# Optimization experiments

Hardware: AMD Instinct MI355X
Metric: run time of the kernel (lower is better)

## Reference

```python
import jax, jax.numpy as jnp
import numpy as np

L, S, B, E, H, FF = 2048, 2048, 4, 1024, 16, 4096
HD = E // H
EPS = 1e-5


def _ln(x, g, b):
    mu = jnp.mean(x, axis=-1, keepdims=True)
    var = jnp.mean(jnp.square(x - mu), axis=-1, keepdims=True)
    return (x - mu) * jax.lax.rsqrt(var + EPS) * g + b


def _mha(xq, xk, xv, Wq, bq, Wk, bk, Wv, bv, Wo, bo, mask):
    l, bsz, e = xq.shape
    s = xk.shape[0]
    q = (xq @ Wq.T + bq).reshape(l, bsz, H, HD)
    k = (xk @ Wk.T + bk).reshape(s, bsz, H, HD)
    v = (xv @ Wv.T + bv).reshape(s, bsz, H, HD)
    scores = jnp.einsum('lbhd,sbhd->bhls', q, k) / (float(HD) ** 0.5)
    if mask is not None:
        scores = scores + mask  # broadcast (L,S) over (B,H,L,S)
    w = jax.nn.softmax(scores, axis=-1)
    out = jnp.einsum('bhls,sbhd->lbhd', w, v).reshape(l, bsz, e)
    return out @ Wo.T + bo


def setup_inputs() -> dict:
    key = jax.random.key(0)
    ks = jax.random.split(key, 32)
    sc = 0.02
    d = {
        'tgt': jax.random.normal(ks[0], (L, B, E), jnp.float32),
        'memory': jax.random.normal(ks[1], (S, B, E), jnp.float32),
        'tgt_mask': jnp.where(jnp.triu(jnp.ones((L, L), bool), k=1), -jnp.inf, 0.0).astype(jnp.float32),
    }
    def lin(i, out_d, in_d):
        return jax.random.normal(ks[i], (out_d, in_d), jnp.float32) * sc, jnp.zeros((out_d,), jnp.float32)
    for pfx, base in (('sa', 2), ('ca', 6)):
        for j, nm in enumerate(('Wq', 'Wk', 'Wv', 'Wo')):
            W, b = lin(base + j, E, E)
            d[f'{pfx}_{nm}'] = W
            d[f'{pfx}_b{nm[1]}'] = b
    d['W1'], d['b1'] = lin(10, FF, E)
    d['W2'], d['b2'] = lin(11, E, FF)
    for i, nm in enumerate(('ln1', 'ln2', 'ln3')):
        d[f'{nm}_g'] = jnp.ones((E,), jnp.float32)
        d[f'{nm}_b'] = jnp.zeros((E,), jnp.float32)
    return d


def reference(tgt, memory, tgt_mask,
              sa_Wq, sa_bq, sa_Wk, sa_bk, sa_Wv, sa_bv, sa_Wo, sa_bo,
              ca_Wq, ca_bq, ca_Wk, ca_bk, ca_Wv, ca_bv, ca_Wo, ca_bo,
              W1, b1, W2, b2,
              ln1_g, ln1_b, ln2_g, ln2_b, ln3_g, ln3_b):
    # masked self-attention + residual + norm1
    sa = _mha(tgt, tgt, tgt, sa_Wq, sa_bq, sa_Wk, sa_bk, sa_Wv, sa_bv, sa_Wo, sa_bo, tgt_mask)
    x = _ln(tgt + sa, ln1_g, ln1_b)
    # cross-attention + residual + norm2
    ca = _mha(x, memory, memory, ca_Wq, ca_bq, ca_Wk, ca_bk, ca_Wv, ca_bv, ca_Wo, ca_bo, None)
    x = _ln(x + ca, ln2_g, ln2_b)
    # FFN + residual + norm3 (dropout = identity in eval)
    ffn = jax.nn.relu(x @ W1.T + b1) @ W2.T + b2
    return _ln(x + ffn, ln3_g, ln3_b)
```

## Files before the change

kernel.cpp:

```cpp
#include <hip/hip_runtime.h>
#include <cstdint>

typedef unsigned short u16;
typedef __bf16 bf16x8 __attribute__((ext_vector_type(8)));
typedef float f32x4 __attribute__((ext_vector_type(4)));

#define L_ 2048
#define S_ 2048
#define B_ 4
#define E_ 1024
#define H_ 16
#define FF_ 4096
#define M_ (L_*B_)

#define QK_SCALE 0.18033688f

__device__ __forceinline__ unsigned f2bf(float f) {
  unsigned u = __float_as_uint(f);
  return (u + 0x7fffu + ((u >> 16) & 1u)) >> 16;
}
__device__ __forceinline__ float bflo(unsigned u){ return __uint_as_float(u << 16); }
__device__ __forceinline__ float bfhi(unsigned u){ return __uint_as_float(u & 0xffff0000u); }

struct CvtSeg { const float* src; u16* dst; int blk_end; };
struct CvtTab { CvtSeg s[6]; };

__global__ __launch_bounds__(256) void cvt_all(CvtTab t, int nseg) {
  const int blk = blockIdx.x;
  int k = 0;
  while (k < nseg - 1 && blk >= t.s[k].blk_end) k++;
  const int b0 = (k == 0) ? 0 : t.s[k-1].blk_end;
  const int off = (blk - b0) * 1024 + threadIdx.x * 4;
  float4 f = *(const float4*)(t.s[k].src + off);
  uint2 u;
  u.x = f2bf(f.x) | (f2bf(f.y) << 16);
  u.y = f2bf(f.z) | (f2bf(f.w) << 16);
  *(uint2*)(t.s[k].dst + off) = u;
}

struct GTab { u16* o[3]; const float* b[3]; float sc[3]; };

__device__ __forceinline__ void gl_lds16(const u16* g, u16* l) {
  __builtin_amdgcn_global_load_lds(
      (const __attribute__((address_space(1))) unsigned int*)g,
      (__attribute__((address_space(3))) unsigned int*)l, 16, 0, 0);
}

#define RAW_BARRIER() do { \
  asm volatile("" ::: "memory"); \
  __builtin_amdgcn_s_barrier(); \
  asm volatile("" ::: "memory"); \
} while (0)

template<int RELU, int NG>
__global__ __launch_bounds__(256, 2) void gemm_bt(
    const u16* __restrict__ A,
    const u16* __restrict__ Bw,
    GTab t, int K, int N)
{
  __shared__ __align__(16) u16 As[128*32];
  __shared__ __align__(16) u16 Bs[128*32];
  const int tid  = threadIdx.x;
  const int lane = tid & 63;
  const int quad = lane >> 4;
  const int l16  = lane & 15;
  const int wave = tid >> 6;
  const int wm = (wave & 1) << 6;
  const int wn = (wave >> 1) << 6;
  const int bm = blockIdx.y << 7;
  const int bn = blockIdx.x << 7;

  const int grp = (NG > 1) ? ((int)blockIdx.x >> 3) : 0;
  u16* Cb = t.o[grp];
  const float* bias = t.b[grp];
  const float scale = t.sc[grp];
  const int ld = (NG > 1) ? 1024 : N;

  const int e0 = tid << 3;
  const int r0 = e0 >> 5;
  const int c0 = e0 & 31;
  const u16* a0 = A  + (size_t)(bm + r0)      * K + c0;
  const u16* a1 = A  + (size_t)(bm + r0 + 64) * K + c0;
  const u16* b0 = Bw + (size_t)(bn + r0)      * K + c0;
  const u16* b1 = Bw + (size_t)(bn + r0 + 64) * K + c0;

  f32x4 acc[4][4];
  #pragma unroll
  for (int i = 0; i < 4; i++)
    #pragma unroll
    for (int j = 0; j < 4; j++)
      acc[i][j] = (f32x4){0.f, 0.f, 0.f, 0.f};

  for (int k0 = 0; k0 < K; k0 += 32) {
    __syncthreads();
    gl_lds16(a0, As + e0);
    gl_lds16(a1, As + e0 + 2048);
    gl_lds16(b0, Bs + e0);
    gl_lds16(b1, Bs + e0 + 2048);
    a0 += 32; a1 += 32; b0 += 32; b1 += 32;
    __syncthreads();

    bf16x8 af[4], bfv[4];
    #pragma unroll
    for (int tt = 0; tt < 4; tt++) {
      af[tt]  = *(const bf16x8*)(As + ((wm + tt*16 + l16) << 5) + (quad << 3));
      bfv[tt] = *(const bf16x8*)(Bs + ((wn + tt*16 + l16) << 5) + (quad << 3));
    }
    #pragma unroll
    for (int mt = 0; mt < 4; mt++)
      #pragma unroll
      for (int nt = 0; nt < 4; nt++)
        acc[mt][nt] = __builtin_amdgcn_mfma_f32_16x16x32_bf16(af[mt], bfv[nt], acc[mt][nt], 0, 0, 0);
  }

  #pragma unroll
  for (int nt = 0; nt < 4; nt++) {
    const int col = bn + wn + nt*16 + l16;
    const int ocol = (NG > 1) ? (col & 1023) : col;
    const float bv = bias[ocol];
    #pragma unroll
    for (int mt = 0; mt < 4; mt++) {
      #pragma unroll
      for (int i = 0; i < 4; i++) {
        const int row = bm + wm + mt*16 + quad*4 + i;
        float v = (acc[mt][nt][i] + bv) * scale;
        if (RELU) v = fmaxf(v, 0.0f);
        Cb[(size_t)row * ld + ocol] = (u16)f2bf(v);
      }
    }
  }
}

template<int RELU, int NG>
__global__ __launch_bounds__(512, 2) void gemm256(
    const u16* __restrict__ A,
    const u16* __restrict__ Bw,
    GTab t, int K, int N)
{
  extern __shared__ __align__(16) u16 LDs[];
  const int tid  = threadIdx.x;
  const int lane = tid & 63;
  const int quad = lane >> 4;
  const int l16  = lane & 15;
  const int w    = tid >> 6;
  const int wm   = w >> 2;
  const int wn   = w & 3;
  const int bm = blockIdx.y << 8;
  const int bn = blockIdx.x << 8;

  const int grp = (NG > 1) ? ((int)blockIdx.x >> 2) : 0;
  u16* Cb = t.o[grp];
  const float* bias = t.b[grp];
  const float scale = t.sc[grp];
  const int ld = (NG > 1) ? 1024 : N;

  const int srow = (w << 4) + (lane >> 2);
  const int cg8  = ((lane & 3) ^ ((lane >> 3) & 3)) << 3;
  const u16* pa0 = A  + (size_t)(bm + srow) * K + cg8;
  const u16* pa1 = pa0 + (size_t)128 * K;
  const u16* pb0 = Bw + (size_t)(bn + srow) * K + cg8;
  const u16* pb1 = pb0 + (size_t)128 * K;
  const int wds = w << 9;

  const int swz  = (quad ^ ((l16 >> 1) & 3)) << 3;
  const int aoff = ((wm << 7) + l16) * 32 + swz;
  const int boff = 8192 + ((wn << 6) + l16) * 32 + swz;

  f32x4 acc[8][4];
  #pragma unroll
  for (int i = 0; i < 8; i++)
    #pragma unroll
    for (int j = 0; j < 4; j++)
      acc[i][j] = (f32x4){0.f, 0.f, 0.f, 0.f};

  const int nk = K >> 5;

  #pragma unroll
  for (int kt = 0; kt < 3; kt++) {
    const int sb = kt << 14;
    gl_lds16(pa0 + kt*32, LDs + sb + wds);
    gl_lds16(pa1 + kt*32, LDs + sb + 4096  + wds);
    gl_lds16(pb0 + kt*32, LDs + sb + 8192  + wds);
    gl_lds16(pb1 + kt*32, LDs + sb + 12288 + wds);
  }
  pa0 += 96; pa1 += 96; pb0 += 96; pb1 += 96;
  asm volatile("s_waitcnt vmcnt(8)" ::: "memory");
  RAW_BARRIER();

  for (int it = 0; it < nk; ++it) {
    const int rb = (it & 3) << 14;
    const int sb = ((it + 3) & 3) << 14;

    bf16x8 bfr[4], afr[4];
    #pragma unroll
    for (int nt = 0; nt < 4; nt++)
      bfr[nt] = *(const bf16x8*)(LDs + rb + boff + nt*512);
    #pragma unroll
    for (int mt = 0; mt < 4; mt++)
      afr[mt] = *(const bf16x8*)(LDs + rb + aoff + mt*512);
    gl_lds16(pa0, LDs + sb + wds);
    gl_lds16(pa1, LDs + sb + 4096 + wds);
    RAW_BARRIER();
    __builtin_amdgcn_s_setprio(1);
    #pragma unroll
    for (int mt = 0; mt < 4; mt++)
      #pragma unroll
      for (int nt = 0; nt < 4; nt++)
        acc[mt][nt] = __builtin_amdgcn_mfma_f32_16x16x32_bf16(afr[mt], bfr[nt], acc[mt][nt], 0, 0, 0);
    __builtin_amdgcn_s_setprio(0);
    RAW_BARRIER();

    #pragma unroll
    for (int mt = 0; mt < 4; mt++)
      afr[mt] = *(const bf16x8*)(LDs + rb + aoff + (4 + mt)*512);
    gl_lds16(pb0, LDs + sb + 8192  + wds);
    gl_lds16(pb1, LDs + sb + 12288 + wds);
    asm volatile("s_waitcnt vmcnt(8)" ::: "memory");
    RAW_BARRIER();
    __builtin_amdgcn_s_setprio(1);
    #pragma unroll
    for (int mt = 0; mt < 4; mt++)
      #pragma unroll
      for (int nt = 0; nt < 4; nt++)
        acc[4 + mt][nt] = __builtin_amdgcn_mfma_f32_16x16x32_bf16(afr[mt], bfr[nt], acc[4 + mt][nt], 0, 0, 0);
    __builtin_amdgcn_s_setprio(0);
    RAW_BARRIER();

    if (it + 4 < nk) { pa0 += 32; pa1 += 32; pb0 += 32; pb1 += 32; }
  }

  #pragma unroll
  for (int nt = 0; nt < 4; nt++) {
    const int col = bn + (wn << 6) + nt*16 + l16;
    const int ocol = (NG > 1) ? (col & 1023) : col;
    const float bv = bias[ocol];
    #pragma unroll
    for (int mt = 0; mt < 8; mt++) {
      #pragma unroll
      for (int i = 0; i < 4; i++) {
        const int row = bm + (wm << 7) + mt*16 + quad*4 + i;
        float v = (acc[mt][nt][i] + bv) * scale;
        if (RELU) v = fmaxf(v, 0.0f);
        Cb[(size_t)row * ld + ocol] = (u16)f2bf(v);
      }
    }
  }
}

__global__ __launch_bounds__(256) void transpose_v(
    const u16* __restrict__ V, u16* __restrict__ Vt)
{
  const int t = threadIdx.x;
  const int lane = t & 63;
  const int w = t >> 6;
  const int bh = blockIdx.y;
  const int b = bh >> 4, h = bh & 15;
  const int l = (blockIdx.x << 6) + lane;
  const size_t vrow = ((size_t)l * B_ + b) * E_ + h * 64;
  #pragma unroll
  for (int g = 0; g < 2; g++) {
    const int d0 = w * 8 + g * 32;
    uint4 u = *(const uint4*)(V + vrow + d0);
    u16 e[8];
    e[0] = u.x & 0xffff; e[1] = u.x >> 16;
    e[2] = u.y & 0xffff; e[3] = u.y >> 16;
    e[4] = u.z & 0xffff; e[5] = u.z >> 16;
    e[6] = u.w & 0xffff; e[7] = u.w >> 16;
    #pragma unroll
    for (int j = 0; j < 8; j++)
      Vt[(size_t)(bh * 64 + d0 + j) * S_ + l] = e[j];
  }
}

template<int CAUSAL>
__global__ __launch_bounds__(256, 4) void attn_mfma(
    const u16* __restrict__ Q,
    const u16* __restrict__ Kg,
    const u16* __restrict__ Vt,
    u16* __restrict__ O,
    int Skv)
{
  __shared__ __align__(16) u16 Tile[16384];
  const int tid  = threadIdx.x;
  const int lane = tid & 63;
  const int w    = tid >> 6;
  const int l16  = lane & 15;
  const int quad = lane >> 4;
  const int bh = blockIdx.x;
  const int b = bh >> 4, h = bh & 15;
  const int y = blockIdx.y;
  const int q0 = (CAUSAL ? ((y < 8) ? (15 - 2*y) : (2*y - 16)) : y) << 7;
  const int wq = q0 + w*32;

  bf16x8 qf[2][2];
  #pragma unroll
  for (int h2 = 0; h2 < 2; h2++) {
    const size_t qoff = ((size_t)(wq + h2*16 + l16) * B_ + b) * E_ + h*64;
    qf[h2][0] = *(const bf16x8*)(Q + qoff + quad*8);
    qf[h2][1] = *(const bf16x8*)(Q + qoff + 32 + quad*8);
  }

  f32x4 oacc[2][4];
  #pragma unroll
  for (int h2 = 0; h2 < 2; h2++)
    #pragma unroll
    for (int i = 0; i < 4; i++) oacc[h2][i] = (f32x4){0.f,0.f,0.f,0.f};
  float lsum[2] = {0.f, 0.f};

  const int lrow = lane >> 3;
  const int lchunk = (lane & 7) ^ lrow;
  const u16* kp = Kg + ((size_t)(16*w + lrow) * B_ + b) * E_ + h*64 + lchunk*8;
  const u16* vp = Vt + (size_t)(bh*64 + 16*w + lrow) * Skv + lchunk*8;
  const size_t kRow8 = (size_t)8 * B_ * E_;
  const size_t kTile = (size_t)64 * B_ * E_;
  u16* ldsK = Tile + w*1024;
  u16* ldsV = Tile + 4096 + w*1024;

  const int pbase = 8192 + w*2048;
  int aKV[2], aW[4];
  #pragma unroll
  for (int kh = 0; kh < 2; kh++)
    aKV[kh] = l16*64 + (((kh*4 + quad) ^ (l16 & 7)) << 3);
  #pragma unroll
  for (int st = 0; st < 4; st++)
    aW[st] = pbase + l16*64 +
             ((((st*2) + (quad >> 1)) ^ (l16 & 7)) << 3) + ((quad & 1) << 2);

  const int send = CAUSAL ? (q0 + 128) : Skv;
  for (int s0 = 0; s0 < send; s0 += 64) {
    __syncthreads();
    gl_lds16(kp,         ldsK);
    gl_lds16(kp + kRow8, ldsK + 512);
    gl_lds16(vp,         ldsV);
    gl_lds16(vp + 8*Skv, ldsV + 512);
    kp += kTile; vp += 64;
    __syncthreads();

    if (CAUSAL && s0 >= wq + 32) continue;

    f32x4 sacc[2][4];
    #pragma unroll
    for (int h2 = 0; h2 < 2; h2++)
      #pragma unroll
      for (int st = 0; st < 4; st++) sacc[h2][st] = (f32x4){0.f,0.f,0.f,0.f};
    #pragma unroll
    for (int kh = 0; kh < 2; kh++)
      #pragma unroll
      for (int st = 0; st < 4; st++) {
        bf16x8 kf = *(const bf16x8*)(Tile + aKV[kh] + st*1024);
        sacc[0][st] = __builtin_amdgcn_mfma_f32_16x16x32_bf16(kf, qf[0][kh], sacc[0][st], 0, 0, 0);
        sacc[1][st] = __builtin_amdgcn_mfma_f32_16x16x32_bf16(kf, qf[1][kh], sacc[1][st], 0, 0, 0);
      }

    #pragma unroll
    for (int h2 = 0; h2 < 2; h2++) {
      float p[16];
      #pragma unroll
      for (int st = 0; st < 4; st++)
        #pragma unroll
        for (int r = 0; r < 4; r++) p[st*4+r] = sacc[h2][st][r];
      if (CAUSAL && s0 + 63 > wq + h2*16) {
        const int qa = wq + h2*16 + l16;
        #pragma unroll
        for (int st = 0; st < 4; st++)
          #pragma unroll
          for (int r = 0; r < 4; r++)
            if (s0 + st*16 + quad*4 + r > qa) p[st*4+r] = -3e38f;
      }
      #pragma unroll
      for (int i = 0; i < 16; i++) p[i] = exp2f(p[i]);
      float s01 = (p[0]+p[1]) + (p[2]+p[3]);
      float s23 = (p[4]+p[5]) + (p[6]+p[7]);
      float s45 = (p[8]+p[9]) + (p[10]+p[11]);
      float s67 = (p[12]+p[13]) + (p[14]+p[15]);
      lsum[h2] += (s01+s23) + (s45+s67);

      #pragma unroll
      for (int st = 0; st < 4; st++) {
        uint2 d;
        d.x = __builtin_amdgcn_perm(__float_as_uint(p[st*4+1]), __float_as_uint(p[st*4+0]), 0x07060302u);
        d.y = __builtin_amdgcn_perm(__float_as_uint(p[st*4+3]), __float_as_uint(p[st*4+2]), 0x07060302u);
        *(uint2*)(Tile + aW[st] + h2*1024) = d;
      }
    }

    #pragma unroll
    for (int kh = 0; kh < 2; kh++) {
      bf16x8 pf[2];
      #pragma unroll
      for (int h2 = 0; h2 < 2; h2++)
        pf[h2] = *(const bf16x8*)(Tile + pbase + h2*1024 + aKV[kh]);
      #pragma unroll
      for (int dt = 0; dt < 4; dt++) {
        bf16x8 vf = *(const bf16x8*)(Tile + 4096 + aKV[kh] + dt*1024);
        #pragma unroll
        for (int h2 = 0; h2 < 2; h2++)
          oacc[h2][dt] = __builtin_amdgcn_mfma_f32_16x16x32_bf16(pf[h2], vf, oacc[h2][dt], 0, 0, 0);
      }
    }
  }

  #pragma unroll
  for (int h2 = 0; h2 < 2; h2++) {
    float rs = lsum[h2];
    rs += __shfl_xor(rs, 16);
    rs += __shfl_xor(rs, 32);
    const float inv = 1.0f / rs;
    #pragma unroll
    for (int r = 0; r < 4; r++) {
      const float li = __shfl(inv, (quad << 2) + r);
      const int qg = wq + h2*16 + quad*4 + r;
      const size_t orow = ((size_t)qg * B_ + b) * E_ + h*64;
      #pragma unroll
      for (int dt = 0; dt < 4; dt++)
        O[orow + dt*16 + l16] = (u16)f2bf(oacc[h2][dt][r] * li);
    }
  }
}

template<int RF32>
__global__ __launch_bounds__(256) void add_ln(
    const u16* __restrict__ X,
    const float* __restrict__ Rf, const u16* __restrict__ Rb,
    const float* __restrict__ g, const float* __restrict__ be,
    float* __restrict__ outF, u16* __restrict__ outB)
{
  const int row = blockIdx.x;
  const int tid = threadIdx.x;
  const size_t base = (size_t)row * E_;
  uint2 xu = *(const uint2*)(X + base + tid*4);
  float x0 = bflo(xu.x), x1 = bfhi(xu.x), x2 = bflo(xu.y), x3 = bfhi(xu.y);
  float r0, r1, r2, r3;
  if (RF32) {
    float4 rv = *(const float4*)(Rf + base + tid*4);
    r0 = rv.x; r1 = rv.y; r2 = rv.z; r3 = rv.w;
  } else {
    uint2 ru = *(const uint2*)(Rb + base + tid*4);
    r0 = bflo(ru.x); r1 = bfhi(ru.x); r2 = bflo(ru.y); r3 = bfhi(ru.y);
  }
  const float v0 = x0 + r0, v1 = x1 + r1, v2 = x2 + r2, v3 = x3 + r3;
  float s  = v0 + v1 + v2 + v3;
  float s2 = v0*v0 + v1*v1 + v2*v2 + v3*v3;
  #pragma unroll
  for (int off = 32; off >= 1; off >>= 1) {
    s  += __shfl_down(s,  off);
    s2 += __shfl_down(s2, off);
  }
  __shared__ float ps[4], ps2[4];
  const int wv = tid >> 6, lane = tid & 63;
  if (lane == 0) { ps[wv] = s; ps2[wv] = s2; }
  __syncthreads();
  const float ts  = ps[0] + ps[1] + ps[2] + ps[3];
  const float ts2 = ps2[0] + ps2[1] + ps2[2] + ps2[3];
  const float mu  = ts * (1.0f / E_);
  const float var = ts2 * (1.0f / E_) - mu * mu;
  const float rsq = rsqrtf(var + 1e-5f);
  float4 gv = *(const float4*)(g  + tid*4);
  float4 bv = *(const float4*)(be + tid*4);
  const float o0 = (v0 - mu) * rsq * gv.x + bv.x;
  const float o1 = (v1 - mu) * rsq * gv.y + bv.y;
  const float o2 = (v2 - mu) * rsq * gv.z + bv.z;
  const float o3 = (v3 - mu) * rsq * gv.w + bv.w;
  if (outF) {
    float4 ov; ov.x = o0; ov.y = o1; ov.z = o2; ov.w = o3;
    *(float4*)(outF + base + tid*4) = ov;
  }
  if (outB) {
    uint2 u;
    u.x = f2bf(o0) | (f2bf(o1) << 16);
    u.y = f2bf(o2) | (f2bf(o3) << 16);
    *(uint2*)(outB + base + tid*4) = u;
  }
}

extern "C" void kernel_launch(void* const* d_in, const int* in_sizes, int n_in,
                              void* d_out, int out_size, void* d_ws, size_t ws_size,
                              hipStream_t stream) {
  (void)in_sizes; (void)n_in; (void)out_size; (void)ws_size;
  const float* tgt  = (const float*)d_in[0];
  const float* mem  = (const float*)d_in[1];
  const float* saWq = (const float*)d_in[3];  const float* sabq = (const float*)d_in[4];
  const float* saWk = (const float*)d_in[5];  const float* sabk = (const float*)d_in[6];
  const float* saWv = (const float*)d_in[7];  const float* sabv = (const float*)d_in[8];
  const float* saWo = (const float*)d_in[9];  const float* sabo = (const float*)d_in[10];
  const float* caWq = (const float*)d_in[11]; const float* cabq = (const float*)d_in[12];
  const float* caWk = (const float*)d_in[13]; const float* cabk = (const float*)d_in[14];
  const float* caWv = (const float*)d_in[15]; const float* cabv = (const float*)d_in[16];
  const float* caWo = (const float*)d_in[17]; const float* cabo = (const float*)d_in[18];
  const float* W1   = (const float*)d_in[19]; const float* b1   = (const float*)d_in[20];
  const float* W2   = (const float*)d_in[21]; const float* b2   = (const float*)d_in[22];
  const float* ln1g = (const float*)d_in[23]; const float* ln1b = (const float*)d_in[24];
  const float* ln2g = (const float*)d_in[25]; const float* ln2b = (const float*)d_in[26];
  const float* ln3g = (const float*)d_in[27]; const float* ln3b = (const float*)d_in[28];
  float* out = (float*)d_out;

  static bool attr_done = false;
  if (!attr_done) {
    (void)hipFuncSetAttribute(reinterpret_cast<const void*>(&gemm256<0,3>),
                              hipFuncAttributeMaxDynamicSharedMemorySize, 131072);
    (void)hipFuncSetAttribute(reinterpret_cast<const void*>(&gemm256<0,2>),
                              hipFuncAttributeMaxDynamicSharedMemorySize, 131072);
    (void)hipFuncSetAttribute(reinterpret_cast<const void*>(&gemm256<1,1>),
                              hipFuncAttributeMaxDynamicSharedMemorySize, 131072);
    attr_done = true;
  }

  char* wsp = (char*)d_ws;
  const size_t MB16 = (size_t)16 * 1024 * 1024;
  u16* A  = (u16*)(wsp + 0 * MB16);
  u16* Cq = (u16*)(wsp + 1 * MB16);
  u16* Bm = (u16*)(wsp + 2 * MB16);
  u16* Dk = (u16*)(wsp + 3 * MB16);
  u16* Ev = (u16*)(wsp + 4 * MB16);
  u16* Ff = (u16*)(wsp + 5 * MB16);
  u16* wS = (u16*)(wsp + 6 * MB16);
  u16* hb = Cq;
  const int MEG = 1024 * 1024;

  dim3 blk(256);
  dim3 blk512(512);
  dim3 g8(8, 64);
  dim3 gQKV256(12, 32);
  dim3 gKV256(8, 32);
  dim3 gFF256(16, 32);
  dim3 ga(B_*H_, L_/128);
  dim3 gt(S_/64, B_*H_);

  auto gt1 = [](u16* o, const float* bi, float s) {
    GTab t{}; t.o[0]=o; t.o[1]=o; t.o[2]=o; t.b[0]=bi; t.b[1]=bi; t.b[2]=bi;
    t.sc[0]=s; t.sc[1]=s; t.sc[2]=s; return t;
  };

  {
    CvtTab t{};
    t.s[0] = {tgt,  A,        8192};
    t.s[1] = {mem,  Bm,       16384};
    t.s[2] = {saWq, wS,       17408};
    t.s[3] = {saWk, wS + MEG,   18432};
    t.s[4] = {saWv, wS + 2*MEG, 19456};
    t.s[5] = {saWo, wS + 3*MEG, 20480};
    cvt_all<<<20480, blk, 0, stream>>>(t, 6);
  }

  {
    GTab t{};
    t.o[0]=Cq; t.o[1]=Dk; t.o[2]=Ev;
    t.b[0]=sabq; t.b[1]=sabk; t.b[2]=sabv;
    t.sc[0]=QK_SCALE; t.sc[1]=1.f; t.sc[2]=1.f;
    gemm256<0,3><<<gQKV256, blk512, 131072, stream>>>(A, wS, t, E_, 3*E_);
  }
  transpose_v<<<gt, blk, 0, stream>>>(Ev, Ff);
  attn_mfma<1><<<ga, blk, 0, stream>>>(Cq, Dk, Ff, Cq, S_);
  gemm_bt<0,1><<<g8, blk, 0, stream>>>(Cq, wS + 3*MEG, gt1(Ff, sabo, 1.f), E_, E_);
  add_ln<1><<<M_, blk, 0, stream>>>(Ff, tgt, nullptr, ln1g, ln1b, nullptr, A);

  {
    CvtTab t{};
    t.s[0] = {caWq, wS,        1024};
    t.s[1] = {caWk, wS + MEG,    2048};
    t.s[2] = {caWv, wS + 2*MEG,  3072};
    t.s[3] = {caWo, wS + 3*MEG,  4096};
    cvt_all<<<4096, blk, 0, stream>>>(t, 4);
  }

  gemm_bt<0,1><<<g8, blk, 0, stream>>>(A, wS, gt1(Cq, cabq, QK_SCALE), E_, E_);
  {
    GTab t{};
    t.o[0]=Dk; t.o[1]=Ev; t.o[2]=Ev;
    t.b[0]=cabk; t.b[1]=cabv; t.b[2]=cabv;
    t.sc[0]=1.f; t.sc[1]=1.f; t.sc[2]=1.f;
    gemm256<0,2><<<gKV256, blk512, 131072, stream>>>(Bm, wS + MEG, t, E_, 2*E_);
  }
  transpose_v<<<gt, blk, 0, stream>>>(Ev, Ff);
  attn_mfma<0><<<ga, blk, 0, stream>>>(Cq, Dk, Ff, Cq, S_);
  gemm_bt<0,1><<<g8, blk, 0, stream>>>(Cq, wS + 3*MEG, gt1(Ff, cabo, 1.f), E_, E_);
  add_ln<0><<<M_, blk, 0, stream>>>(Ff, nullptr, A, ln2g, ln2b, nullptr, A);

  {
    CvtTab t{};
    t.s[0] = {W1, wS, 4096};
    cvt_all<<<4096, blk, 0, stream>>>(t, 1);
  }
  gemm256<1,1><<<gFF256, blk512, 131072, stream>>>(A, wS, gt1(hb, b1, 1.f), E_, FF_);
  {
    CvtTab t{};
    t.s[0] = {W2, wS, 4096};
    cvt_all<<<4096, blk, 0, stream>>>(t, 1);
  }
  gemm_bt<0,1><<<g8, blk, 0, stream>>>(hb, wS, gt1(Ff, b2, 1.f), FF_, E_);
  add_ln<0><<<M_, blk, 0, stream>>>(Ff, nullptr, A, ln3g, ln3b, out, nullptr);
}
```

Baseline: 824.3 us.

## Replace N=1024 GEMMs with pipelined 256x128 tile kernel using swizzled LDS

Swaps the simple 128x128 single-buffered gemm_bt kernel, used for the output projections, the cross-attention Q projection and the FFN down-projection, for a new 256x128 tile kernel with 512 threads. The new kernel keeps a three-stage ring of LDS buffers filled asynchronously with global_load_lds, XOR-swizzles the LDS layout to avoid bank conflicts, and splits each k-step into two MFMA phases with setprio. The aim is to hide global-load latency behind the matrix math and cut the per-k-step barrier stalls of the old kernel. The larger tile halves the grid to 256 blocks, which may leave some compute units underused.

```diff
diff --git a/kernel.cpp b/kernel.cpp
--- a/kernel.cpp
+++ b/kernel.cpp
@@ -51,85 +51,6 @@
   __builtin_amdgcn_s_barrier(); \
   asm volatile("" ::: "memory"); \
 } while (0)
-
-template<int RELU, int NG>
-__global__ __launch_bounds__(256, 2) void gemm_bt(
-    const u16* __restrict__ A,
-    const u16* __restrict__ Bw,
-    GTab t, int K, int N)
-{
-  __shared__ __align__(16) u16 As[128*32];
-  __shared__ __align__(16) u16 Bs[128*32];
-  const int tid  = threadIdx.x;
-  const int lane = tid & 63;
-  const int quad = lane >> 4;
-  const int l16  = lane & 15;
-  const int wave = tid >> 6;
-  const int wm = (wave & 1) << 6;
-  const int wn = (wave >> 1) << 6;
-  const int bm = blockIdx.y << 7;
-  const int bn = blockIdx.x << 7;
-
-  const int grp = (NG > 1) ? ((int)blockIdx.x >> 3) : 0;
-  u16* Cb = t.o[grp];
-  const float* bias = t.b[grp];
-  const float scale = t.sc[grp];
-  const int ld = (NG > 1) ? 1024 : N;
-
-  const int e0 = tid << 3;
-  const int r0 = e0 >> 5;
-  const int c0 = e0 & 31;
-  const u16* a0 = A  + (size_t)(bm + r0)      * K + c0;
-  const u16* a1 = A  + (size_t)(bm + r0 + 64) * K + c0;
-  const u16* b0 = Bw + (size_t)(bn + r0)      * K + c0;
-  const u16* b1 = Bw + (size_t)(bn + r0 + 64) * K + c0;
-
-  f32x4 acc[4][4];
-  #pragma unroll
-  for (int i = 0; i < 4; i++)
-    #pragma unroll
-    for (int j = 0; j < 4; j++)
-      acc[i][j] = (f32x4){0.f, 0.f, 0.f, 0.f};
-
-  for (int k0 = 0; k0 < K; k0 += 32) {
-    __syncthreads();
-    gl_lds16(a0, As + e0);
-    gl_lds16(a1, As + e0 + 2048);
-    gl_lds16(b0, Bs + e0);
-    gl_lds16(b1, Bs + e0 + 2048);
-    a0 += 32; a1 += 32; b0 += 32; b1 += 32;
-    __syncthreads();
-
-    bf16x8 af[4], bfv[4];
-    #pragma unroll
-    for (int tt = 0; tt < 4; tt++) {
-      af[tt]  = *(const bf16x8*)(As + ((wm + tt*16 + l16) << 5) + (quad << 3));
-      bfv[tt] = *(const bf16x8*)(Bs + ((wn + tt*16 + l16) << 5) + (quad << 3));
-    }
-    #pragma unroll
-    for (int mt = 0; mt < 4; mt++)
-      #pragma unroll
-      for (int nt = 0; nt < 4; nt++)
-        acc[mt][nt] = __builtin_amdgcn_mfma_f32_16x16x32_bf16(af[mt], bfv[nt], acc[mt][nt], 0, 0, 0);
-  }
-
-  #pragma unroll
-  for (int nt = 0; nt < 4; nt++) {
-    const int col = bn + wn + nt*16 + l16;
-    const int ocol = (NG > 1) ? (col & 1023) : col;
-    const float bv = bias[ocol];
-    #pragma unroll
-    for (int mt = 0; mt < 4; mt++) {
-      #pragma unroll
-      for (int i = 0; i < 4; i++) {
-        const int row = bm + wm + mt*16 + quad*4 + i;
-        float v = (acc[mt][nt][i] + bv) * scale;
-        if (RELU) v = fmaxf(v, 0.0f);
-        Cb[(size_t)row * ld + ocol] = (u16)f2bf(v);
-      }
-    }
-  }
-}
 
 template<int RELU, int NG>
 __global__ __launch_bounds__(512, 2) void gemm256(
@@ -242,6 +163,112 @@
         float v = (acc[mt][nt][i] + bv) * scale;
         if (RELU) v = fmaxf(v, 0.0f);
         Cb[(size_t)row * ld + ocol] = (u16)f2bf(v);
+      }
+    }
+  }
+}
+
+template<int RELU>
+__global__ __launch_bounds__(512, 2) void gemm256n(
+    const u16* __restrict__ A,
+    const u16* __restrict__ Bw,
+    const float* __restrict__ bias,
+    u16* __restrict__ C,
+    float scale, int K, int N)
+{
+  extern __shared__ __align__(16) u16 LDs[];
+  const int tid  = threadIdx.x;
+  const int lane = tid & 63;
+  const int quad = lane >> 4;
+  const int l16  = lane & 15;
+  const int w    = tid >> 6;
+  const int wm   = w >> 1;
+  const int wn   = w & 1;
+  const int bm = blockIdx.y << 8;
+  const int bn = blockIdx.x << 7;
+
+  const int srow = (w << 4) + (lane >> 2);
+  const int cg8  = ((lane & 3) ^ ((lane >> 3) & 3)) << 3;
+  const u16* pa0 = A  + (size_t)(bm + srow) * K + cg8;
+  const u16* pa1 = pa0 + (size_t)128 * K;
+  const u16* pb0 = Bw + (size_t)(bn + srow) * K + cg8;
+  const int wds = w << 9;
+
+  const int swz  = (quad ^ ((l16 >> 1) & 3)) << 3;
+  const int aoff = ((wm << 6) + l16) * 32 + swz;
+  const int boff = 8192 + ((wn << 6) + l16) * 32 + swz;
+
+  f32x4 acc[4][4];
+  #pragma unroll
+  for (int i = 0; i < 4; i++)
+    #pragma unroll
+    for (int j = 0; j < 4; j++)
+      acc[i][j] = (f32x4){0.f, 0.f, 0.f, 0.f};
+
+  const int nk = K >> 5;
+
+  #pragma unroll
+  for (int kt = 0; kt < 2; kt++) {
+    const int sb = kt * 12288;
+    gl_lds16(pa0 + kt*32, LDs + sb + wds);
+    gl_lds16(pa1 + kt*32, LDs + sb + 4096 + wds);
+    gl_lds16(pb0 + kt*32, LDs + sb + 8192 + wds);
+  }
+  pa0 += 64; pa1 += 64; pb0 += 64;
+  asm volatile("s_waitcnt vmcnt(3)" ::: "memory");
+  RAW_BARRIER();
+
+  int rb = 0, sb = 24576;
+  for (int it = 0; it < nk; ++it) {
+    bf16x8 bfr[4], afr0, afr1;
+    #pragma unroll
+    for (int nt = 0; nt < 4; nt++)
+      bfr[nt] = *(const bf16x8*)(LDs + rb + boff + nt*512);
+    afr0 = *(const bf16x8*)(LDs + rb + aoff);
+    afr1 = *(const bf16x8*)(LDs + rb + aoff + 512);
+    gl_lds16(pa0, LDs + sb + wds);
+    gl_lds16(pa1, LDs + sb + 4096 + wds);
+    RAW_BARRIER();
+    __builtin_amdgcn_s_setprio(1);
+    #pragma unroll
+    for (int nt = 0; nt < 4; nt++) {
+      acc[0][nt] = __builtin_amdgcn_mfma_f32_16x16x32_bf16(afr0, bfr[nt], acc[0][nt], 0, 0, 0);
+      acc[1][nt] = __builtin_amdgcn_mfma_f32_16x16x32_bf16(afr1, bfr[nt], acc[1][nt], 0, 0, 0);
+    }
+    __builtin_amdgcn_s_setprio(0);
+    RAW_BARRIER();
+
+    afr0 = *(const bf16x8*)(LDs + rb + aoff + 1024);
+    afr1 = *(const bf16x8*)(LDs + rb + aoff + 1536);
+    gl_lds16(pb0, LDs + sb + 8192 + wds);
+    asm volatile("s_waitcnt vmcnt(3)" ::: "memory");
+    RAW_BARRIER();
+    __builtin_amdgcn_s_setprio(1);
+    #pragma unroll
+    for (int nt = 0; nt < 4; nt++) {
+      acc[2][nt] = __builtin_amdgcn_mfma_f32_16x16x32_bf16(afr0, bfr[nt], acc[2][nt], 0, 0, 0);
+      acc[3][nt] = __builtin_amdgcn_mfma_f32_16x16x32_bf16(afr1, bfr[nt], acc[3][nt], 0, 0, 0);
+    }
+    __builtin_amdgcn_s_setprio(0);
+    RAW_BARRIER();
+
+    if (it + 3 < nk) { pa0 += 32; pa1 += 32; pb0 += 32; }
+    rb += 12288; if (rb == 36864) rb = 0;
+    sb += 12288; if (sb == 36864) sb = 0;
+  }
+
+  #pragma unroll
+  for (int nt = 0; nt < 4; nt++) {
+    const int col = bn + (wn << 6) + nt*16 + l16;
+    const float bv = bias[col];
+    #pragma unroll
+    for (int mt = 0; mt < 4; mt++) {
+      #pragma unroll
+      for (int i = 0; i < 4; i++) {
+        const int row = bm + (wm << 6) + mt*16 + quad*4 + i;
+        float v = (acc[mt][nt][i] + bv) * scale;
+        if (RELU) v = fmaxf(v, 0.0f);
+        C[(size_t)row * N + col] = (u16)f2bf(v);
       }
     }
   }
@@ -502,6 +529,8 @@
                               hipFuncAttributeMaxDynamicSharedMemorySize, 131072);
     (void)hipFuncSetAttribute(reinterpret_cast<const void*>(&gemm256<1,1>),
                               hipFuncAttributeMaxDynamicSharedMemorySize, 131072);
+    (void)hipFuncSetAttribute(reinterpret_cast<const void*>(&gemm256n<0>),
+                              hipFuncAttributeMaxDynamicSharedMemorySize, 73728);
     attr_done = true;
   }
 
@@ -519,17 +548,12 @@
 
   dim3 blk(256);
   dim3 blk512(512);
-  dim3 g8(8, 64);
+  dim3 gN1(8, 32);
   dim3 gQKV256(12, 32);
   dim3 gKV256(8, 32);
   dim3 gFF256(16, 32);
   dim3 ga(B_*H_, L_/128);
   dim3 gt(S_/64, B_*H_);
-
-  auto gt1 = [](u16* o, const float* bi, float s) {
-    GTab t{}; t.o[0]=o; t.o[1]=o; t.o[2]=o; t.b[0]=bi; t.b[1]=bi; t.b[2]=bi;
-    t.sc[0]=s; t.sc[1]=s; t.sc[2]=s; return t;
-  };
 
   {
     CvtTab t{};
@@ -551,7 +575,7 @@
   }
   transpose_v<<<gt, blk, 0, stream>>>(Ev, Ff);
   attn_mfma<1><<<ga, blk, 0, stream>>>(Cq, Dk, Ff, Cq, S_);
-  gemm_bt<0,1><<<g8, blk, 0, stream>>>(Cq, wS + 3*MEG, gt1(Ff, sabo, 1.f), E_, E_);
+  gemm256n<0><<<gN1, blk512, 73728, stream>>>(Cq, wS + 3*MEG, sabo, Ff, 1.f, E_, E_);
   add_ln<1><<<M_, blk, 0, stream>>>(Ff, tgt, nullptr, ln1g, ln1b, nullptr, A);
 
   {
@@ -563,7 +587,7 @@
     cvt_all<<<4096, blk, 0, stream>>>(t, 4);
   }
 
-  gemm_bt<0,1><<<g8, blk, 0, stream>>>(A, wS, gt1(Cq, cabq, QK_SCALE), E_, E_);
+  gemm256n<0><<<gN1, blk512, 73728, stream>>>(A, wS, cabq, Cq, QK_SCALE, E_, E_);
   {
     GTab t{};
     t.o[0]=Dk; t.o[1]=Ev; t.o[2]=Ev;
@@ -573,7 +597,7 @@
   }
   transpose_v<<<gt, blk, 0, stream>>>(Ev, Ff);
   attn_mfma<0><<<ga, blk, 0, stream>>>(Cq, Dk, Ff, Cq, S_);
-  gemm_bt<0,1><<<g8, blk, 0, stream>>>(Cq, wS + 3*MEG, gt1(Ff, cabo, 1.f), E_, E_);
+  gemm256n<0><<<gN1, blk512, 73728, stream>>>(Cq, wS + 3*MEG, cabo, Ff, 1.f, E_, E_);
   add_ln<0><<<M_, blk, 0, stream>>>(Ff, nullptr, A, ln2g, ln2b, nullptr, A);
 
   {
@@ -581,12 +605,18 @@
     t.s[0] = {W1, wS, 4096};
     cvt_all<<<4096, blk, 0, stream>>>(t, 1);
   }
-  gemm256<1,1><<<gFF256, blk512, 131072, stream>>>(A, wS, gt1(hb, b1, 1.f), E_, FF_);
+  {
+    GTab t{};
+    t.o[0]=hb; t.o[1]=hb; t.o[2]=hb;
+    t.b[0]=b1; t.b[1]=b1; t.b[2]=b1;
+    t.sc[0]=1.f; t.sc[1]=1.f; t.sc[2]=1.f;
+    gemm256<1,1><<<gFF256, blk512, 131072, stream>>>(A, wS, t, E_, FF_);
+  }
   {
     CvtTab t{};
     t.s[0] = {W2, wS, 4096};
     cvt_all<<<4096, blk, 0, stream>>>(t, 1);
   }
-  gemm_bt<0,1><<<g8, blk, 0, stream>>>(hb, wS, gt1(Ff, b2, 1.f), FF_, E_);
+  gemm256n<0><<<gN1, blk512, 73728, stream>>>(hb, wS, b2, Ff, 1.f, FF_, E_);
   add_ln<0><<<M_, blk, 0, stream>>>(Ff, nullptr, A, ln3g, ln3b, out, nullptr);
 }
```

New measurement: 810.4 us. Within noise of the previous version (-1.7%).
